# Optimization experiments

Measured on AMD Instinct MI355X. Metric: run time of the kernel, lower is better.

## Reference

```python
import jax, jax.numpy as jnp
import numpy as np

N_EMBED = 8192
EMB_DIM = 32
BETA = 1.0
DECAY = 0.99
N_TOKENS = 32768


def l2norm(x, axis=-1):
    # matches torch F.normalize(p=2, dim=-1, eps=1e-12)
    n = jnp.sqrt(jnp.sum(x * x, axis=axis, keepdims=True))
    return x / jnp.maximum(n, 1e-12)


def setup_inputs() -> dict:
    key = jax.random.key(0)
    k1, k2 = jax.random.split(key)
    z = jax.random.normal(k1, (N_TOKENS, EMB_DIM), dtype=jnp.float32)
    weight = l2norm(jax.random.normal(k2, (N_EMBED, EMB_DIM), dtype=jnp.float32))
    cluster_size = jnp.zeros((N_EMBED,), dtype=jnp.float32)
    return {"z": z, "weight": weight, "cluster_size": cluster_size}


def reference(z, weight, cluster_size):
    z = l2norm(z)  # [B, D]
    # pairwise squared L2 distances: [B, N]
    d = (jnp.sum(z * z, axis=1, keepdims=True)
         + jnp.sum(weight * weight, axis=1)
         - 2.0 * jnp.einsum('bd,nd->bn', z, weight))
    encoding_indices = jnp.argmin(d, axis=1)  # [B]
    z_q = weight[encoding_indices]            # gather, [B, D]

    # training-branch EMA updates (expressed functionally)
    bins = jnp.zeros((N_EMBED,), z.dtype).at[encoding_indices].add(1.0)
    new_cluster_size = cluster_size * DECAY + bins * (1.0 - DECAY)
    zero_mask = bins == 0
    safe_bins = jnp.where(zero_mask, 1.0, bins)
    # embed_sum = z^T @ one_hot(idx) done as a scatter-add: [N, D]
    embed_sum = jnp.zeros((N_EMBED, EMB_DIM), z.dtype).at[encoding_indices].add(z)
    embed_normalized = l2norm(embed_sum / safe_bins[:, None])
    embed_normalized = jnp.where(zero_mask[:, None], weight, embed_normalized)
    new_weight = l2norm(weight * DECAY + embed_normalized * (1.0 - DECAY))

    # commitment loss: z_q detached vs z
    loss = BETA * jnp.mean((jax.lax.stop_gradient(z_q) - z) ** 2)
    # straight-through estimator
    z_q_st = z + jax.lax.stop_gradient(z_q - z)
    return z_q_st, loss, encoding_indices, new_weight, new_cluster_size
```

## Files before the change

### kernel.cpp

```cpp
#include <hip/hip_runtime.h>
#include <math.h>

#define N_TOKENS 32768
#define N_EMBED  8192
#define EMB      32
#define DECAYF   0.99f
#define OMDF     0.01f

#define WS_WW    0
#define WS_ENC   (WS_WW + N_EMBED)
#define WS_BINS  (WS_ENC + N_TOKENS)
#define WS_ESUM  (WS_BINS + N_EMBED)
#define WS_LOSS  (WS_ESUM + N_EMBED*EMB)

#define OUT_ZQ   0
#define OUT_LOSS (N_TOKENS*EMB)
#define OUT_IDX  (OUT_LOSS + 1)
#define OUT_NW   (OUT_IDX + N_TOKENS)
#define OUT_CS   (OUT_NW + N_EMBED*EMB)

__global__ void k_prep(const float* __restrict__ z, const float* __restrict__ w,
                       float* __restrict__ zn, float* __restrict__ ww) {
    int t = blockIdx.x * blockDim.x + threadIdx.x;
    if (t < N_TOKENS) {
        const float4* zp = (const float4*)(z + (size_t)t * EMB);
        float4 v[8];
        float acc = 0.f;
#pragma unroll
        for (int i = 0; i < 8; ++i) {
            v[i] = zp[i];
            acc += v[i].x * v[i].x + v[i].y * v[i].y + v[i].z * v[i].z + v[i].w * v[i].w;
        }
        float n = fmaxf(sqrtf(acc), 1e-12f);
        float4* o = (float4*)(zn + (size_t)t * EMB);
#pragma unroll
        for (int i = 0; i < 8; ++i) {
            float4 r;
            r.x = v[i].x / n; r.y = v[i].y / n; r.z = v[i].z / n; r.w = v[i].w / n;
            o[i] = r;
        }
    } else if (t < N_TOKENS + N_EMBED) {
        int r = t - N_TOKENS;
        const float4* wp = (const float4*)(w + (size_t)r * EMB);
        float acc = 0.f;
#pragma unroll
        for (int i = 0; i < 8; ++i) {
            float4 v = wp[i];
            acc += v.x * v.x + v.y * v.y + v.z * v.z + v.w * v.w;
        }
        ww[r] = acc;
    }
}

#define SLICES 8
#define ROWS_PER_SLICE (N_EMBED / SLICES)

__global__ __launch_bounds__(512) void k_argmin(const float* __restrict__ zn,
                                                const float* __restrict__ weight,
                                                const float* __restrict__ ww,
                                                int* __restrict__ enc) {
    __shared__ float sBest[SLICES][64];
    __shared__ int   sIdx[SLICES][64];

    const int lane = threadIdx.x & 63;
    const int wv   = __builtin_amdgcn_readfirstlane(threadIdx.x >> 6);
    const int token = blockIdx.x * 64 + lane;

    float zr[EMB];
    const float4* zp = (const float4*)(zn + (size_t)token * EMB);
#pragma unroll
    for (int i = 0; i < 8; ++i) {
        float4 v = zp[i];
        zr[4 * i + 0] = v.x; zr[4 * i + 1] = v.y; zr[4 * i + 2] = v.z; zr[4 * i + 3] = v.w;
    }

    const int n0 = wv * ROWS_PER_SLICE;
    const float* wrow  = weight + (size_t)n0 * EMB;
    const float* wwrow = ww + n0;

    float best = 3.4e38f;
    int bidx = 0;

#pragma unroll 4
    for (int i = 0; i < ROWS_PER_SLICE; ++i) {
        const float4* wp = (const float4*)(wrow + (size_t)i * EMB);
        float a0 = 0.f, a1 = 0.f;
#pragma unroll
        for (int k = 0; k < 8; ++k) {
            float4 w4 = wp[k];
            a0 = fmaf(zr[4 * k + 0], w4.x, a0);
            a1 = fmaf(zr[4 * k + 1], w4.y, a1);
            a0 = fmaf(zr[4 * k + 2], w4.z, a0);
            a1 = fmaf(zr[4 * k + 3], w4.w, a1);
        }
        float key = fmaf(-2.f, a0 + a1, wwrow[i]);
        bool c = key < best;
        best = c ? key : best;
        bidx = c ? (n0 + i) : bidx;
    }

    sBest[wv][lane] = best;
    sIdx[wv][lane]  = bidx;
    __syncthreads();

    if (wv == 0) {
        float b = sBest[0][lane];
        int   bi = sIdx[0][lane];
#pragma unroll
        for (int s = 1; s < SLICES; ++s) {
            float ob = sBest[s][lane];
            int   oi = sIdx[s][lane];
            bool c = ob < b;
            b  = c ? ob : b;
            bi = c ? oi : bi;
        }
        enc[token] = bi;
    }
}

__global__ void k_token(const float* __restrict__ weight,
                        const int* __restrict__ enc, float* __restrict__ out,
                        float* __restrict__ bins, float* __restrict__ esum,
                        float* __restrict__ loss) {
    int t = blockIdx.x * blockDim.x + threadIdx.x;
    int idx = enc[t];
    float4* zq = (float4*)(out + OUT_ZQ + (size_t)t * EMB);
    const float4* wp = (const float4*)(weight + (size_t)idx * EMB);

    float lacc = 0.f;
#pragma unroll
    for (int i = 0; i < 8; ++i) {
        float4 zv = zq[i];
        float4 wv = wp[i];
        float4 d, o;
        d.x = wv.x - zv.x; d.y = wv.y - zv.y; d.z = wv.z - zv.z; d.w = wv.w - zv.w;
        lacc += d.x * d.x + d.y * d.y + d.z * d.z + d.w * d.w;
        o.x = zv.x + d.x; o.y = zv.y + d.y; o.z = zv.z + d.z; o.w = zv.w + d.w;
        zq[i] = o;
        atomicAdd(esum + (size_t)idx * EMB + 4 * i + 0, zv.x);
        atomicAdd(esum + (size_t)idx * EMB + 4 * i + 1, zv.y);
        atomicAdd(esum + (size_t)idx * EMB + 4 * i + 2, zv.z);
        atomicAdd(esum + (size_t)idx * EMB + 4 * i + 3, zv.w);
    }
    out[OUT_IDX + t] = (float)idx;
    atomicAdd(bins + idx, 1.0f);

#pragma unroll
    for (int off = 32; off > 0; off >>= 1) lacc += __shfl_xor(lacc, off, 64);
    if ((threadIdx.x & 63) == 0) atomicAdd(loss, lacc);
}

__global__ void k_ema(const float* __restrict__ weight, const float* __restrict__ cs,
                      const float* __restrict__ bins, const float* __restrict__ esum,
                      const float* __restrict__ loss, float* __restrict__ out) {
    int n = blockIdx.x * blockDim.x + threadIdx.x;
    if (n == 0) {
        out[OUT_LOSS] = loss[0] * (1.0f / (float)(N_TOKENS * EMB));
    }
    if (n >= N_EMBED) return;

    float b = bins[n];
    out[OUT_CS + n] = cs[n] * DECAYF + b * OMDF;

    bool zero = (b == 0.0f);
    float safe = zero ? 1.0f : b;

    float w[EMB], en[EMB];
    const float* wrow = weight + (size_t)n * EMB;
    const float* erow = esum + (size_t)n * EMB;
    float nacc = 0.f;
#pragma unroll
    for (int i = 0; i < EMB; ++i) {
        w[i] = wrow[i];
        en[i] = erow[i] / safe;
        nacc += en[i] * en[i];
    }
    float nn = fmaxf(sqrtf(nacc), 1e-12f);
#pragma unroll
    for (int i = 0; i < EMB; ++i) {
        en[i] = zero ? w[i] : (en[i] / nn);
    }
    float acc2 = 0.f;
    float nw[EMB];
#pragma unroll
    for (int i = 0; i < EMB; ++i) {
        nw[i] = w[i] * DECAYF + en[i] * OMDF;
        acc2 += nw[i] * nw[i];
    }
    float n2 = fmaxf(sqrtf(acc2), 1e-12f);
#pragma unroll
    for (int i = 0; i < EMB; ++i) {
        out[OUT_NW + (size_t)n * EMB + i] = nw[i] / n2;
    }
}

extern "C" void kernel_launch(void* const* d_in, const int* in_sizes, int n_in,
                              void* d_out, int out_size, void* d_ws, size_t ws_size,
                              hipStream_t stream) {
    const float* z  = (const float*)d_in[0];
    const float* w  = (const float*)d_in[1];
    const float* cs = (const float*)d_in[2];
    float* out = (float*)d_out;
    float* ws  = (float*)d_ws;

    float* zn   = out + OUT_ZQ;
    float* ww   = ws + WS_WW;
    int*   enc  = (int*)(ws + WS_ENC);
    float* bins = ws + WS_BINS;
    float* esum = ws + WS_ESUM;
    float* loss = ws + WS_LOSS;

    hipMemsetAsync(bins, 0, (size_t)(N_EMBED + N_EMBED * EMB + 1) * sizeof(float), stream);

    k_prep<<<(N_TOKENS + N_EMBED + 255) / 256, 256, 0, stream>>>(z, w, zn, ww);
    k_argmin<<<N_TOKENS / 64, 512, 0, stream>>>(zn, w, ww, enc);
    k_token<<<N_TOKENS / 256, 256, 0, stream>>>(w, enc, out, bins, esum, loss);
    k_ema<<<(N_EMBED + 255) / 256, 256, 0, stream>>>(w, cs, bins, esum, loss, out);
}
```

Measured before the change: 396.8 us.

## Register-block two tokens per thread in argmin and fuse z normalization

The argmin kernel now has each lane handle two tokens, so every codebook row it loads feeds twice as many FMAs, halving codebook load traffic per token. The block grows to 1024 threads split into 16 codebook slices. Token L2 normalization moves from the prep kernel into the argmin kernel, where wave 0 writes zn, and the prep kernel shrinks to computing codebook norms. The cost is higher register pressure from two 32-float token vectors per thread, which may reduce occupancy under launch_bounds(1024,4).

```diff
diff --git a/kernel.cpp b/kernel.cpp
--- a/kernel.cpp
+++ b/kernel.cpp
@@ -19,102 +19,122 @@
 #define OUT_NW   (OUT_IDX + N_TOKENS)
 #define OUT_CS   (OUT_NW + N_EMBED*EMB)
 
-__global__ void k_prep(const float* __restrict__ z, const float* __restrict__ w,
-                       float* __restrict__ zn, float* __restrict__ ww) {
-    int t = blockIdx.x * blockDim.x + threadIdx.x;
-    if (t < N_TOKENS) {
-        const float4* zp = (const float4*)(z + (size_t)t * EMB);
-        float4 v[8];
-        float acc = 0.f;
-#pragma unroll
-        for (int i = 0; i < 8; ++i) {
-            v[i] = zp[i];
-            acc += v[i].x * v[i].x + v[i].y * v[i].y + v[i].z * v[i].z + v[i].w * v[i].w;
-        }
-        float n = fmaxf(sqrtf(acc), 1e-12f);
-        float4* o = (float4*)(zn + (size_t)t * EMB);
-#pragma unroll
-        for (int i = 0; i < 8; ++i) {
-            float4 r;
-            r.x = v[i].x / n; r.y = v[i].y / n; r.z = v[i].z / n; r.w = v[i].w / n;
-            o[i] = r;
-        }
-    } else if (t < N_TOKENS + N_EMBED) {
-        int r = t - N_TOKENS;
-        const float4* wp = (const float4*)(w + (size_t)r * EMB);
-        float acc = 0.f;
-#pragma unroll
-        for (int i = 0; i < 8; ++i) {
-            float4 v = wp[i];
-            acc += v.x * v.x + v.y * v.y + v.z * v.z + v.w * v.w;
-        }
-        ww[r] = acc;
-    }
-}
-
-#define SLICES 8
+__global__ void k_ww(const float* __restrict__ w, float* __restrict__ ww) {
+    int r = blockIdx.x * blockDim.x + threadIdx.x;
+    if (r >= N_EMBED) return;
+    const float4* wp = (const float4*)(w + (size_t)r * EMB);
+    float acc = 0.f;
+#pragma unroll
+    for (int i = 0; i < 8; ++i) {
+        float4 v = wp[i];
+        acc += v.x * v.x + v.y * v.y + v.z * v.z + v.w * v.w;
+    }
+    ww[r] = acc;
+}
+
+#define SLICES 16
 #define ROWS_PER_SLICE (N_EMBED / SLICES)
-
-__global__ __launch_bounds__(512) void k_argmin(const float* __restrict__ zn,
-                                                const float* __restrict__ weight,
-                                                const float* __restrict__ ww,
-                                                int* __restrict__ enc) {
-    __shared__ float sBest[SLICES][64];
-    __shared__ int   sIdx[SLICES][64];
+#define TOK_PER_BLOCK  128
+
+__global__ __launch_bounds__(1024, 4) void k_argmin(
+        const float* __restrict__ z, const float* __restrict__ weight,
+        const float* __restrict__ ww, int* __restrict__ enc,
+        float* __restrict__ zn) {
+    __shared__ float sBest[SLICES][2][64];
+    __shared__ int   sIdx[SLICES][2][64];
 
     const int lane = threadIdx.x & 63;
     const int wv   = __builtin_amdgcn_readfirstlane(threadIdx.x >> 6);
-    const int token = blockIdx.x * 64 + lane;
-
-    float zr[EMB];
-    const float4* zp = (const float4*)(zn + (size_t)token * EMB);
-#pragma unroll
-    for (int i = 0; i < 8; ++i) {
-        float4 v = zp[i];
-        zr[4 * i + 0] = v.x; zr[4 * i + 1] = v.y; zr[4 * i + 2] = v.z; zr[4 * i + 3] = v.w;
-    }
-
-    const int n0 = wv * ROWS_PER_SLICE;
-    const float* wrow  = weight + (size_t)n0 * EMB;
-    const float* wwrow = ww + n0;
-
-    float best = 3.4e38f;
-    int bidx = 0;
+    const int tok0 = blockIdx.x * TOK_PER_BLOCK + lane;
+    const int tok1 = tok0 + 64;
+
+    float zr0[EMB], zr1[EMB];
+    {
+        const float4* zp0 = (const float4*)(z + (size_t)tok0 * EMB);
+        const float4* zp1 = (const float4*)(z + (size_t)tok1 * EMB);
+        float acc0 = 0.f, acc1 = 0.f;
+#pragma unroll
+        for (int i = 0; i < 8; ++i) {
+            float4 v0 = zp0[i];
+            float4 v1 = zp1[i];
+            acc0 += v0.x * v0.x + v0.y * v0.y + v0.z * v0.z + v0.w * v0.w;
+            acc1 += v1.x * v1.x + v1.y * v1.y + v1.z * v1.z + v1.w * v1.w;
+            zr0[4*i+0] = v0.x; zr0[4*i+1] = v0.y; zr0[4*i+2] = v0.z; zr0[4*i+3] = v0.w;
+            zr1[4*i+0] = v1.x; zr1[4*i+1] = v1.y; zr1[4*i+2] = v1.z; zr1[4*i+3] = v1.w;
+        }
+        float n0 = fmaxf(sqrtf(acc0), 1e-12f);
+        float n1 = fmaxf(sqrtf(acc1), 1e-12f);
+#pragma unroll
+        for (int k = 0; k < EMB; ++k) { zr0[k] = zr0[k] / n0; zr1[k] = zr1[k] / n1; }
+    }
+#pragma unroll
+    for (int k = 0; k < EMB; ++k) {
+        asm volatile("" : "+v"(zr0[k]));
+        asm volatile("" : "+v"(zr1[k]));
+    }
+
+    if (wv == 0) {
+        float4* o0 = (float4*)(zn + (size_t)tok0 * EMB);
+        float4* o1 = (float4*)(zn + (size_t)tok1 * EMB);
+#pragma unroll
+        for (int i = 0; i < 8; ++i) {
+            float4 a, b;
+            a.x = zr0[4*i+0]; a.y = zr0[4*i+1]; a.z = zr0[4*i+2]; a.w = zr0[4*i+3];
+            b.x = zr1[4*i+0]; b.y = zr1[4*i+1]; b.z = zr1[4*i+2]; b.w = zr1[4*i+3];
+            o0[i] = a; o1[i] = b;
+        }
+    }
+
+    const int n0r = wv * ROWS_PER_SLICE;
+    const float* wrow  = weight + (size_t)n0r * EMB;
+    const float* wwrow = ww + n0r;
+
+    float best0 = 3.4e38f, best1 = 3.4e38f;
+    int bidx0 = 0, bidx1 = 0;
 
 #pragma unroll 4
     for (int i = 0; i < ROWS_PER_SLICE; ++i) {
         const float4* wp = (const float4*)(wrow + (size_t)i * EMB);
-        float a0 = 0.f, a1 = 0.f;
+        float a00 = 0.f, a01 = 0.f, a10 = 0.f, a11 = 0.f;
 #pragma unroll
         for (int k = 0; k < 8; ++k) {
             float4 w4 = wp[k];
-            a0 = fmaf(zr[4 * k + 0], w4.x, a0);
-            a1 = fmaf(zr[4 * k + 1], w4.y, a1);
-            a0 = fmaf(zr[4 * k + 2], w4.z, a0);
-            a1 = fmaf(zr[4 * k + 3], w4.w, a1);
-        }
-        float key = fmaf(-2.f, a0 + a1, wwrow[i]);
-        bool c = key < best;
-        best = c ? key : best;
-        bidx = c ? (n0 + i) : bidx;
-    }
-
-    sBest[wv][lane] = best;
-    sIdx[wv][lane]  = bidx;
+            a00 = fmaf(zr0[4*k+0], w4.x, a00);
+            a01 = fmaf(zr0[4*k+1], w4.y, a01);
+            a10 = fmaf(zr1[4*k+0], w4.x, a10);
+            a11 = fmaf(zr1[4*k+1], w4.y, a11);
+            a00 = fmaf(zr0[4*k+2], w4.z, a00);
+            a01 = fmaf(zr0[4*k+3], w4.w, a01);
+            a10 = fmaf(zr1[4*k+2], w4.z, a10);
+            a11 = fmaf(zr1[4*k+3], w4.w, a11);
+        }
+        float wwv = wwrow[i];
+        float key0 = fmaf(-2.f, a00 + a01, wwv);
+        float key1 = fmaf(-2.f, a10 + a11, wwv);
+        bool c0 = key0 < best0;
+        bool c1 = key1 < best1;
+        best0 = c0 ? key0 : best0;  bidx0 = c0 ? (n0r + i) : bidx0;
+        best1 = c1 ? key1 : best1;  bidx1 = c1 ? (n0r + i) : bidx1;
+    }
+
+    sBest[wv][0][lane] = best0;  sIdx[wv][0][lane] = bidx0;
+    sBest[wv][1][lane] = best1;  sIdx[wv][1][lane] = bidx1;
     __syncthreads();
 
-    if (wv == 0) {
-        float b = sBest[0][lane];
-        int   bi = sIdx[0][lane];
+    if (threadIdx.x < 2 * 64) {
+        const int l = threadIdx.x & 63;
+        const int t = threadIdx.x >> 6;
+        float b = sBest[0][t][l];
+        int   bi = sIdx[0][t][l];
 #pragma unroll
         for (int s = 1; s < SLICES; ++s) {
-            float ob = sBest[s][lane];
-            int   oi = sIdx[s][lane];
+            float ob = sBest[s][t][l];
+            int   oi = sIdx[s][t][l];
             bool c = ob < b;
             b  = c ? ob : b;
             bi = c ? oi : bi;
         }
-        enc[token] = bi;
+        enc[blockIdx.x * TOK_PER_BLOCK + t * 64 + l] = bi;
     }
 }
 
@@ -212,8 +232,8 @@
 
     hipMemsetAsync(bins, 0, (size_t)(N_EMBED + N_EMBED * EMB + 1) * sizeof(float), stream);
 
-    k_prep<<<(N_TOKENS + N_EMBED + 255) / 256, 256, 0, stream>>>(z, w, zn, ww);
-    k_argmin<<<N_TOKENS / 64, 512, 0, stream>>>(zn, w, ww, enc);
+    k_ww<<<N_EMBED / 256, 256, 0, stream>>>(w, ww);
+    k_argmin<<<N_TOKENS / TOK_PER_BLOCK, 1024, 0, stream>>>(z, w, ww, enc, zn);
     k_token<<<N_TOKENS / 256, 256, 0, stream>>>(w, enc, out, bins, esum, loss);
     k_ema<<<(N_EMBED + 255) / 256, 256, 0, stream>>>(w, cs, bins, esum, loss, out);
 }
```

Measured after the change: 357.0 us. 10.0% less time.

## Restructure argmin so each lane holds a codebook row and waves share 16 tokens

Applied to the files above, without the earlier changes.

The argmin kernel is reorganised. Each lane now keeps one codebook row in registers, and each wave loops over all codebook chunks for 16 tokens whose normalized values are read as wave-uniform (scalar) loads. Weight rows are double-buffered in registers so the next chunk loads while the current one is computed, and per-token winners are reduced with cross-lane shuffles, with a tie-break on lower index. The normalized z is moved into the workspace and the weight-norm computation gets its own kernel. The goal is to cut the per-token reloading of the whole codebook and raise arithmetic reuse, at the cost of much higher register pressure from the waves_per_eu(2,2) hint and far fewer blocks.

```diff
diff --git a/kernel.cpp b/kernel.cpp
--- a/kernel.cpp
+++ b/kernel.cpp
@@ -7,7 +7,8 @@
 #define DECAYF   0.99f
 #define OMDF     0.01f
 
-#define WS_WW    0
+#define WS_ZN    0
+#define WS_WW    (N_TOKENS*EMB)
 #define WS_ENC   (WS_WW + N_EMBED)
 #define WS_BINS  (WS_ENC + N_TOKENS)
 #define WS_ESUM  (WS_BINS + N_EMBED)
@@ -19,124 +20,142 @@
 #define OUT_NW   (OUT_IDX + N_TOKENS)
 #define OUT_CS   (OUT_NW + N_EMBED*EMB)
 
-__global__ void k_prep(const float* __restrict__ z, const float* __restrict__ w,
-                       float* __restrict__ zn, float* __restrict__ ww) {
+__global__ void k_prep(const float* __restrict__ z, float* __restrict__ zn) {
     int t = blockIdx.x * blockDim.x + threadIdx.x;
-    if (t < N_TOKENS) {
-        const float4* zp = (const float4*)(z + (size_t)t * EMB);
-        float4 v[8];
-        float acc = 0.f;
-#pragma unroll
-        for (int i = 0; i < 8; ++i) {
-            v[i] = zp[i];
-            acc += v[i].x * v[i].x + v[i].y * v[i].y + v[i].z * v[i].z + v[i].w * v[i].w;
-        }
-        float n = fmaxf(sqrtf(acc), 1e-12f);
-        float4* o = (float4*)(zn + (size_t)t * EMB);
-#pragma unroll
-        for (int i = 0; i < 8; ++i) {
-            float4 r;
-            r.x = v[i].x / n; r.y = v[i].y / n; r.z = v[i].z / n; r.w = v[i].w / n;
-            o[i] = r;
-        }
-    } else if (t < N_TOKENS + N_EMBED) {
-        int r = t - N_TOKENS;
-        const float4* wp = (const float4*)(w + (size_t)r * EMB);
-        float acc = 0.f;
-#pragma unroll
-        for (int i = 0; i < 8; ++i) {
-            float4 v = wp[i];
-            acc += v.x * v.x + v.y * v.y + v.z * v.z + v.w * v.w;
-        }
-        ww[r] = acc;
-    }
-}
-
-#define SLICES 8
-#define ROWS_PER_SLICE (N_EMBED / SLICES)
-
-__global__ __launch_bounds__(512) void k_argmin(const float* __restrict__ zn,
-                                                const float* __restrict__ weight,
-                                                const float* __restrict__ ww,
-                                                int* __restrict__ enc) {
-    __shared__ float sBest[SLICES][64];
-    __shared__ int   sIdx[SLICES][64];
-
+    const float4* zp = (const float4*)(z + (size_t)t * EMB);
+    float4 v[8];
+    float acc = 0.f;
+#pragma unroll
+    for (int i = 0; i < 8; ++i) {
+        v[i] = zp[i];
+        acc += v[i].x * v[i].x + v[i].y * v[i].y + v[i].z * v[i].z + v[i].w * v[i].w;
+    }
+    float n = fmaxf(sqrtf(acc), 1e-12f);
+    float4* o = (float4*)(zn + (size_t)t * EMB);
+#pragma unroll
+    for (int i = 0; i < 8; ++i) {
+        float4 r;
+        r.x = v[i].x / n; r.y = v[i].y / n; r.z = v[i].z / n; r.w = v[i].w / n;
+        o[i] = r;
+    }
+}
+
+__global__ void k_ww(const float* __restrict__ w, float* __restrict__ ww) {
+    int r = blockIdx.x * blockDim.x + threadIdx.x;
+    if (r >= N_EMBED) return;
+    const float4* wp = (const float4*)(w + (size_t)r * EMB);
+    float acc = 0.f;
+#pragma unroll
+    for (int i = 0; i < 8; ++i) {
+        float4 v = wp[i];
+        acc += v.x * v.x + v.y * v.y + v.z * v.z + v.w * v.w;
+    }
+    ww[r] = acc;
+}
+
+#define TOKS_PER_WAVE 16
+#define WAVES_PER_BLOCK 8
+#define CHUNKS (N_EMBED / 64)
+
+#define LOADW(BUF, CC) do {                                                    \
+    const float4* wp_ = (const float4*)(weight + ((size_t)((CC) * 64 + lane)) * EMB); \
+    _Pragma("unroll")                                                          \
+    for (int q_ = 0; q_ < 8; ++q_) {                                           \
+        float4 v_ = wp_[q_];                                                   \
+        BUF[4*q_+0] = v_.x; BUF[4*q_+1] = v_.y;                                \
+        BUF[4*q_+2] = v_.z; BUF[4*q_+3] = v_.w;                                \
+    }                                                                          \
+} while (0)
+
+#define COMPUTE(W, WWV, CC) do {                                               \
+    const int rowbase_ = (CC) * 64 + lane;                                     \
+    _Pragma("unroll")                                                          \
+    for (int t_ = 0; t_ < TOKS_PER_WAVE; ++t_) {                               \
+        const float* zt_ = zb + t_ * EMB;                                      \
+        float d0_ = 0.f, d1_ = 0.f, d2_ = 0.f, d3_ = 0.f;                      \
+        _Pragma("unroll")                                                      \
+        for (int k_ = 0; k_ < 8; ++k_) {                                       \
+            d0_ = fmaf(W[4*k_+0], zt_[4*k_+0], d0_);                           \
+            d1_ = fmaf(W[4*k_+1], zt_[4*k_+1], d1_);                           \
+            d2_ = fmaf(W[4*k_+2], zt_[4*k_+2], d2_);                           \
+            d3_ = fmaf(W[4*k_+3], zt_[4*k_+3], d3_);                           \
+        }                                                                      \
+        float key_ = fmaf(-2.f, (d0_ + d1_) + (d2_ + d3_), WWV);               \
+        bool c_ = key_ < best[t_];           \
+        best[t_] = c_ ? key_ : best[t_];                                       \
+        bidx[t_] = c_ ? rowbase_ : bidx[t_];                                   \
+    }                                                                          \
+} while (0)
+
+__global__ __attribute__((amdgpu_flat_work_group_size(512, 512),
+                          amdgpu_waves_per_eu(2, 2)))
+void k_argmin(const float* __restrict__ zn, const float* __restrict__ weight,
+              const float* __restrict__ ww, int* __restrict__ enc) {
     const int lane = threadIdx.x & 63;
     const int wv   = __builtin_amdgcn_readfirstlane(threadIdx.x >> 6);
-    const int token = blockIdx.x * 64 + lane;
-
-    float zr[EMB];
-    const float4* zp = (const float4*)(zn + (size_t)token * EMB);
-#pragma unroll
-    for (int i = 0; i < 8; ++i) {
-        float4 v = zp[i];
-        zr[4 * i + 0] = v.x; zr[4 * i + 1] = v.y; zr[4 * i + 2] = v.z; zr[4 * i + 3] = v.w;
-    }
-
-    const int n0 = wv * ROWS_PER_SLICE;
-    const float* wrow  = weight + (size_t)n0 * EMB;
-    const float* wwrow = ww + n0;
-
-    float best = 3.4e38f;
-    int bidx = 0;
-
-#pragma unroll 4
-    for (int i = 0; i < ROWS_PER_SLICE; ++i) {
-        const float4* wp = (const float4*)(wrow + (size_t)i * EMB);
-        float a0 = 0.f, a1 = 0.f;
-#pragma unroll
-        for (int k = 0; k < 8; ++k) {
-            float4 w4 = wp[k];
-            a0 = fmaf(zr[4 * k + 0], w4.x, a0);
-            a1 = fmaf(zr[4 * k + 1], w4.y, a1);
-            a0 = fmaf(zr[4 * k + 2], w4.z, a0);
-            a1 = fmaf(zr[4 * k + 3], w4.w, a1);
+    const int wid  = blockIdx.x * WAVES_PER_BLOCK + wv;
+    const int tok0 = wid * TOKS_PER_WAVE;
+    const float* zb = zn + (size_t)tok0 * EMB;
+
+    float best[TOKS_PER_WAVE];
+    int   bidx[TOKS_PER_WAVE];
+#pragma unroll
+    for (int t = 0; t < TOKS_PER_WAVE; ++t) { best[t] = 3.4e38f; bidx[t] = 0; }
+
+    float wA[32], wB[32];
+    float wwA, wwB;
+
+    LOADW(wA, 0);
+    wwA = ww[lane];
+
+#pragma unroll 1
+    for (int c = 0; c < CHUNKS; c += 2) {
+        LOADW(wB, c + 1);
+        wwB = ww[(c + 1) * 64 + lane];
+        COMPUTE(wA, wwA, c);
+
+        const int cn = (c + 2 < CHUNKS) ? (c + 2) : 0;
+        LOADW(wA, cn);
+        wwA = ww[cn * 64 + lane];
+        COMPUTE(wB, wwB, c + 1);
+    }
+
+#pragma unroll
+    for (int t = 0; t < TOKS_PER_WAVE; ++t) {
+        float b = best[t];
+        int   bi = bidx[t];
+#pragma unroll
+        for (int off = 32; off >= 1; off >>= 1) {
+            float ob = __shfl_xor(b, off, 64);
+            int   oi = __shfl_xor(bi, off, 64);
+            bool c2 = (ob < b) || (ob == b && oi < bi);
+            b  = c2 ? ob : b;
+            bi = c2 ? oi : bi;
         }
-        float key = fmaf(-2.f, a0 + a1, wwrow[i]);
-        bool c = key < best;
-        best = c ? key : best;
-        bidx = c ? (n0 + i) : bidx;
-    }
-
-    sBest[wv][lane] = best;
-    sIdx[wv][lane]  = bidx;
-    __syncthreads();
-
-    if (wv == 0) {
-        float b = sBest[0][lane];
-        int   bi = sIdx[0][lane];
-#pragma unroll
-        for (int s = 1; s < SLICES; ++s) {
-            float ob = sBest[s][lane];
-            int   oi = sIdx[s][lane];
-            bool c = ob < b;
-            b  = c ? ob : b;
-            bi = c ? oi : bi;
-        }
-        enc[token] = bi;
-    }
-}
-
-__global__ void k_token(const float* __restrict__ weight,
+        if (lane == 0) enc[tok0 + t] = bi;
+    }
+}
+
+__global__ void k_token(const float* __restrict__ zn, const float* __restrict__ weight,
                         const int* __restrict__ enc, float* __restrict__ out,
                         float* __restrict__ bins, float* __restrict__ esum,
                         float* __restrict__ loss) {
     int t = blockIdx.x * blockDim.x + threadIdx.x;
     int idx = enc[t];
-    float4* zq = (float4*)(out + OUT_ZQ + (size_t)t * EMB);
+    const float4* zp = (const float4*)(zn + (size_t)t * EMB);
     const float4* wp = (const float4*)(weight + (size_t)idx * EMB);
+    float4* oq = (float4*)(out + OUT_ZQ + (size_t)t * EMB);
 
     float lacc = 0.f;
 #pragma unroll
     for (int i = 0; i < 8; ++i) {
-        float4 zv = zq[i];
+        float4 zv = zp[i];
         float4 wv = wp[i];
         float4 d, o;
         d.x = wv.x - zv.x; d.y = wv.y - zv.y; d.z = wv.z - zv.z; d.w = wv.w - zv.w;
         lacc += d.x * d.x + d.y * d.y + d.z * d.z + d.w * d.w;
         o.x = zv.x + d.x; o.y = zv.y + d.y; o.z = zv.z + d.z; o.w = zv.w + d.w;
-        zq[i] = o;
+        oq[i] = o;
         atomicAdd(esum + (size_t)idx * EMB + 4 * i + 0, zv.x);
         atomicAdd(esum + (size_t)idx * EMB + 4 * i + 1, zv.y);
         atomicAdd(esum + (size_t)idx * EMB + 4 * i + 2, zv.z);
@@ -203,7 +222,7 @@
     float* out = (float*)d_out;
     float* ws  = (float*)d_ws;
 
-    float* zn   = out + OUT_ZQ;
+    float* zn   = ws + WS_ZN;
     float* ww   = ws + WS_WW;
     int*   enc  = (int*)(ws + WS_ENC);
     float* bins = ws + WS_BINS;
@@ -212,8 +231,9 @@
 
     hipMemsetAsync(bins, 0, (size_t)(N_EMBED + N_EMBED * EMB + 1) * sizeof(float), stream);
 
-    k_prep<<<(N_TOKENS + N_EMBED + 255) / 256, 256, 0, stream>>>(z, w, zn, ww);
-    k_argmin<<<N_TOKENS / 64, 512, 0, stream>>>(zn, w, ww, enc);
-    k_token<<<N_TOKENS / 256, 256, 0, stream>>>(w, enc, out, bins, esum, loss);
+    k_prep<<<N_TOKENS / 256, 256, 0, stream>>>(z, zn);
+    k_ww<<<N_EMBED / 256, 256, 0, stream>>>(w, ww);
+    k_argmin<<<N_TOKENS / (TOKS_PER_WAVE * WAVES_PER_BLOCK), 512, 0, stream>>>(zn, w, ww, enc);
+    k_token<<<N_TOKENS / 256, 256, 0, stream>>>(zn, w, enc, out, bins, esum, loss);
     k_ema<<<(N_EMBED + 255) / 256, 256, 0, stream>>>(w, cs, bins, esum, loss, out);
 }
```

Result: slower. 881.7 us (+122.2%).

## Use split-bf16 MFMA distance scan with exact fp32 candidate re-check

Applied to the files above, without the earlier changes.

Replaces the scalar fp32 argmin over all codebook rows with a matrix-core scan that uses hi/lo bf16 splits (three MFMAs per tile) to approximate the dot products. A first pass picks an approximate best index. An exact fp32 key for that index then sets a per-token threshold, and a second scan records every candidate within epsilon of it. The candidates are re-scored exactly and merged with a packed 64-bit atomicMin. This trades the full fp32 FMA workload for two MFMA passes plus a small exact correction. It adds risk from the candidate buffer cap, atomic contention, and the epsilon margin being enough to preserve exact argmin ties.

```diff
diff --git a/kernel.cpp b/kernel.cpp
--- a/kernel.cpp
+++ b/kernel.cpp
@@ -6,12 +6,23 @@
 #define EMB      32
 #define DECAYF   0.99f
 #define OMDF     0.01f
-
-#define WS_WW    0
-#define WS_ENC   (WS_WW + N_EMBED)
-#define WS_BINS  (WS_ENC + N_TOKENS)
-#define WS_ESUM  (WS_BINS + N_EMBED)
-#define WS_LOSS  (WS_ESUM + N_EMBED*EMB)
+#define EPSK     2e-4f
+#define CAND_CAP 65536
+
+typedef unsigned short ushortT;
+typedef __attribute__((ext_vector_type(8))) short short8;
+typedef __attribute__((ext_vector_type(4))) float f32x4;
+
+#define WS_WHI  0
+#define WS_WLO  (WS_WHI + 131072)
+#define WS_WWN  (WS_WLO + 131072)
+#define WS_THR  (WS_WWN + N_EMBED)
+#define WS_PACK (WS_THR + N_TOKENS)
+#define WS_BINS (WS_PACK + 2*N_TOKENS)
+#define WS_ESUM (WS_BINS + N_EMBED)
+#define WS_LOSS (WS_ESUM + N_EMBED*EMB)
+#define WS_CCNT (WS_LOSS + 1)
+#define WS_CAND (WS_CCNT + 1)
 
 #define OUT_ZQ   0
 #define OUT_LOSS (N_TOKENS*EMB)
@@ -19,132 +30,272 @@
 #define OUT_NW   (OUT_IDX + N_TOKENS)
 #define OUT_CS   (OUT_NW + N_EMBED*EMB)
 
-__global__ void k_prep(const float* __restrict__ z, const float* __restrict__ w,
-                       float* __restrict__ zn, float* __restrict__ ww) {
-    int t = blockIdx.x * blockDim.x + threadIdx.x;
-    if (t < N_TOKENS) {
-        const float4* zp = (const float4*)(z + (size_t)t * EMB);
-        float4 v[8];
-        float acc = 0.f;
-#pragma unroll
-        for (int i = 0; i < 8; ++i) {
-            v[i] = zp[i];
-            acc += v[i].x * v[i].x + v[i].y * v[i].y + v[i].z * v[i].z + v[i].w * v[i].w;
-        }
-        float n = fmaxf(sqrtf(acc), 1e-12f);
-        float4* o = (float4*)(zn + (size_t)t * EMB);
-#pragma unroll
-        for (int i = 0; i < 8; ++i) {
-            float4 r;
-            r.x = v[i].x / n; r.y = v[i].y / n; r.z = v[i].z / n; r.w = v[i].w / n;
-            o[i] = r;
-        }
-    } else if (t < N_TOKENS + N_EMBED) {
-        int r = t - N_TOKENS;
-        const float4* wp = (const float4*)(w + (size_t)r * EMB);
-        float acc = 0.f;
-#pragma unroll
-        for (int i = 0; i < 8; ++i) {
-            float4 v = wp[i];
-            acc += v.x * v.x + v.y * v.y + v.z * v.z + v.w * v.w;
-        }
-        ww[r] = acc;
-    }
-}
-
-#define SLICES 8
-#define ROWS_PER_SLICE (N_EMBED / SLICES)
-
-__global__ __launch_bounds__(512) void k_argmin(const float* __restrict__ zn,
-                                                const float* __restrict__ weight,
-                                                const float* __restrict__ ww,
-                                                int* __restrict__ enc) {
-    __shared__ float sBest[SLICES][64];
-    __shared__ int   sIdx[SLICES][64];
-
-    const int lane = threadIdx.x & 63;
-    const int wv   = __builtin_amdgcn_readfirstlane(threadIdx.x >> 6);
-    const int token = blockIdx.x * 64 + lane;
-
-    float zr[EMB];
-    const float4* zp = (const float4*)(zn + (size_t)token * EMB);
+__device__ __forceinline__ ushortT bf16rn(float x) {
+    unsigned b = __float_as_uint(x);
+    unsigned r = (b + 0x7FFFu + ((b >> 16) & 1u)) >> 16;
+    return (ushortT)r;
+}
+__device__ __forceinline__ float bf16tof(ushortT u) {
+    return __uint_as_float(((unsigned)u) << 16);
+}
+__device__ __forceinline__ void load_zn_row(const float* __restrict__ z, int t, float* zr) {
+    const float4* zp = (const float4*)(z + (size_t)t * EMB);
+    float acc = 0.f;
 #pragma unroll
     for (int i = 0; i < 8; ++i) {
         float4 v = zp[i];
-        zr[4 * i + 0] = v.x; zr[4 * i + 1] = v.y; zr[4 * i + 2] = v.z; zr[4 * i + 3] = v.w;
-    }
-
-    const int n0 = wv * ROWS_PER_SLICE;
-    const float* wrow  = weight + (size_t)n0 * EMB;
-    const float* wwrow = ww + n0;
-
-    float best = 3.4e38f;
-    int bidx = 0;
-
-#pragma unroll 4
-    for (int i = 0; i < ROWS_PER_SLICE; ++i) {
-        const float4* wp = (const float4*)(wrow + (size_t)i * EMB);
-        float a0 = 0.f, a1 = 0.f;
-#pragma unroll
-        for (int k = 0; k < 8; ++k) {
-            float4 w4 = wp[k];
-            a0 = fmaf(zr[4 * k + 0], w4.x, a0);
-            a1 = fmaf(zr[4 * k + 1], w4.y, a1);
-            a0 = fmaf(zr[4 * k + 2], w4.z, a0);
-            a1 = fmaf(zr[4 * k + 3], w4.w, a1);
+        zr[4*i+0] = v.x; zr[4*i+1] = v.y; zr[4*i+2] = v.z; zr[4*i+3] = v.w;
+        acc += v.x*v.x + v.y*v.y + v.z*v.z + v.w*v.w;
+    }
+    float n = fmaxf(sqrtf(acc), 1e-12f);
+#pragma unroll
+    for (int k = 0; k < EMB; ++k) zr[k] = zr[k] / n;
+}
+__device__ __forceinline__ float exact_key(const float* zr, const float* __restrict__ wrow, float ww) {
+    float d0 = 0.f, d1 = 0.f, d2 = 0.f, d3 = 0.f;
+#pragma unroll
+    for (int k = 0; k < 8; ++k) {
+        d0 = fmaf(zr[4*k+0], wrow[4*k+0], d0);
+        d1 = fmaf(zr[4*k+1], wrow[4*k+1], d1);
+        d2 = fmaf(zr[4*k+2], wrow[4*k+2], d2);
+        d3 = fmaf(zr[4*k+3], wrow[4*k+3], d3);
+    }
+    return fmaf(-2.f, (d0 + d1) + (d2 + d3), ww);
+}
+__device__ __forceinline__ unsigned long long packkey(float k, int idx) {
+    unsigned u = __float_as_uint(k);
+    u = (u & 0x80000000u) ? ~u : (u | 0x80000000u);
+    return (((unsigned long long)u) << 32) | (unsigned)idx;
+}
+
+__global__ void k_prep(const float* __restrict__ z, ushortT* __restrict__ zhi,
+                       ushortT* __restrict__ zlo) {
+    int t = blockIdx.x * blockDim.x + threadIdx.x;
+    float zr[EMB];
+    load_zn_row(z, t, zr);
+    unsigned h[16], l[16];
+#pragma unroll
+    for (int i = 0; i < 16; ++i) {
+        ushortT h0 = bf16rn(zr[2*i]), h1 = bf16rn(zr[2*i+1]);
+        float r0 = zr[2*i] - bf16tof(h0), r1 = zr[2*i+1] - bf16tof(h1);
+        ushortT l0 = bf16rn(r0), l1 = bf16rn(r1);
+        h[i] = (unsigned)h0 | ((unsigned)h1 << 16);
+        l[i] = (unsigned)l0 | ((unsigned)l1 << 16);
+    }
+    uint4* dh = (uint4*)(zhi + (size_t)t * EMB);
+    uint4* dl = (uint4*)(zlo + (size_t)t * EMB);
+#pragma unroll
+    for (int q = 0; q < 4; ++q) {
+        dh[q] = make_uint4(h[4*q], h[4*q+1], h[4*q+2], h[4*q+3]);
+        dl[q] = make_uint4(l[4*q], l[4*q+1], l[4*q+2], l[4*q+3]);
+    }
+}
+
+__global__ void k_wprep(const float* __restrict__ w, ushortT* __restrict__ whi,
+                        ushortT* __restrict__ wlo, float* __restrict__ wwn) {
+    int r = blockIdx.x * blockDim.x + threadIdx.x;
+    if (r >= N_EMBED) return;
+    const float4* wp = (const float4*)(w + (size_t)r * EMB);
+    float wr[EMB];
+    float acc = 0.f;
+#pragma unroll
+    for (int i = 0; i < 8; ++i) {
+        float4 v = wp[i];
+        wr[4*i+0] = v.x; wr[4*i+1] = v.y; wr[4*i+2] = v.z; wr[4*i+3] = v.w;
+        acc += v.x*v.x + v.y*v.y + v.z*v.z + v.w*v.w;
+    }
+    wwn[r] = -0.5f * acc;
+    unsigned h[16], l[16];
+#pragma unroll
+    for (int i = 0; i < 16; ++i) {
+        ushortT h0 = bf16rn(wr[2*i]), h1 = bf16rn(wr[2*i+1]);
+        float r0 = wr[2*i] - bf16tof(h0), r1 = wr[2*i+1] - bf16tof(h1);
+        ushortT l0 = bf16rn(r0), l1 = bf16rn(r1);
+        h[i] = (unsigned)h0 | ((unsigned)h1 << 16);
+        l[i] = (unsigned)l0 | ((unsigned)l1 << 16);
+    }
+    uint4* dh = (uint4*)(whi + (size_t)r * EMB);
+    uint4* dl = (uint4*)(wlo + (size_t)r * EMB);
+#pragma unroll
+    for (int q = 0; q < 4; ++q) {
+        dh[q] = make_uint4(h[4*q], h[4*q+1], h[4*q+2], h[4*q+3]);
+        dl[q] = make_uint4(l[4*q], l[4*q+1], l[4*q+2], l[4*q+3]);
+    }
+}
+
+template<int MODE>
+__global__ __launch_bounds__(256) void k_scan(
+        const ushortT* __restrict__ zhi, const ushortT* __restrict__ zlo,
+        const ushortT* __restrict__ whi, const ushortT* __restrict__ wlo,
+        const float* __restrict__ wwn, const float* __restrict__ thr,
+        unsigned long long* __restrict__ packed,
+        unsigned* __restrict__ ccnt, unsigned long long* __restrict__ cand) {
+    const int lane = threadIdx.x & 63;
+    const int wv   = threadIdx.x >> 6;
+    const int wid  = blockIdx.x * 4 + wv;
+    const int tok0 = wid * 32;
+    const int l15  = lane & 15;
+    const int lg   = lane >> 4;
+
+    const size_t aoff0 = ((size_t)(tok0 + l15)) * EMB + 8 * lg;
+    const size_t aoff1 = ((size_t)(tok0 + 16 + l15)) * EMB + 8 * lg;
+    const short8 a0h = *(const short8*)(zhi + aoff0);
+    const short8 a0l = *(const short8*)(zlo + aoff0);
+    const short8 a1h = *(const short8*)(zhi + aoff1);
+    const short8 a1l = *(const short8*)(zlo + aoff1);
+
+    float best0[4], best1[4];
+    int   bid0[4], bid1[4];
+    float thrv0[4], thrv1[4];
+    if (MODE == 0) {
+#pragma unroll
+        for (int r = 0; r < 4; ++r) {
+            best0[r] = -3.4e38f; best1[r] = -3.4e38f; bid0[r] = 0; bid1[r] = 0;
         }
-        float key = fmaf(-2.f, a0 + a1, wwrow[i]);
-        bool c = key < best;
-        best = c ? key : best;
-        bidx = c ? (n0 + i) : bidx;
-    }
-
-    sBest[wv][lane] = best;
-    sIdx[wv][lane]  = bidx;
-    __syncthreads();
-
-    if (wv == 0) {
-        float b = sBest[0][lane];
-        int   bi = sIdx[0][lane];
-#pragma unroll
-        for (int s = 1; s < SLICES; ++s) {
-            float ob = sBest[s][lane];
-            int   oi = sIdx[s][lane];
-            bool c = ob < b;
-            b  = c ? ob : b;
-            bi = c ? oi : bi;
+    } else {
+#pragma unroll
+        for (int r = 0; r < 4; ++r) {
+            thrv0[r] = thr[tok0 + lg * 4 + r];
+            thrv1[r] = thr[tok0 + 16 + lg * 4 + r];
         }
-        enc[token] = bi;
-    }
-}
-
-__global__ void k_token(const float* __restrict__ weight,
-                        const int* __restrict__ enc, float* __restrict__ out,
-                        float* __restrict__ bins, float* __restrict__ esum,
-                        float* __restrict__ loss) {
+    }
+
+    int vn = l15;
+#pragma unroll 2
+    for (int nt = 0; nt < N_EMBED / 16; ++nt) {
+        const size_t boff = ((size_t)(nt * 16 + l15)) * EMB + 8 * lg;
+        const short8 bh = *(const short8*)(whi + boff);
+        const short8 bl = *(const short8*)(wlo + boff);
+        const float cv = wwn[nt * 16 + l15];
+        f32x4 c0 = {cv, cv, cv, cv};
+        f32x4 c1 = {cv, cv, cv, cv};
+        c0 = __builtin_amdgcn_mfma_f32_16x16x32_bf16(a0l, bh, c0, 0, 0, 0);
+        c0 = __builtin_amdgcn_mfma_f32_16x16x32_bf16(a0h, bl, c0, 0, 0, 0);
+        c0 = __builtin_amdgcn_mfma_f32_16x16x32_bf16(a0h, bh, c0, 0, 0, 0);
+        c1 = __builtin_amdgcn_mfma_f32_16x16x32_bf16(a1l, bh, c1, 0, 0, 0);
+        c1 = __builtin_amdgcn_mfma_f32_16x16x32_bf16(a1h, bl, c1, 0, 0, 0);
+        c1 = __builtin_amdgcn_mfma_f32_16x16x32_bf16(a1h, bh, c1, 0, 0, 0);
+
+        if (MODE == 0) {
+#pragma unroll
+            for (int r = 0; r < 4; ++r) {
+                bool g0 = c0[r] > best0[r];
+                best0[r] = g0 ? c0[r] : best0[r];
+                bid0[r]  = g0 ? vn : bid0[r];
+                bool g1 = c1[r] > best1[r];
+                best1[r] = g1 ? c1[r] : best1[r];
+                bid1[r]  = g1 ? vn : bid1[r];
+            }
+        } else {
+            float k0[4], k1[4];
+#pragma unroll
+            for (int r = 0; r < 4; ++r) { k0[r] = -2.f * c0[r]; k1[r] = -2.f * c1[r]; }
+            bool f = (k0[0] <= thrv0[0]) | (k0[1] <= thrv0[1]) | (k0[2] <= thrv0[2]) |
+                     (k0[3] <= thrv0[3]) | (k1[0] <= thrv1[0]) | (k1[1] <= thrv1[1]) |
+                     (k1[2] <= thrv1[2]) | (k1[3] <= thrv1[3]);
+            if (f) {
+#pragma unroll
+                for (int r = 0; r < 4; ++r) {
+                    if (k0[r] <= thrv0[r]) {
+                        unsigned slot = atomicAdd(ccnt, 1u);
+                        if (slot < CAND_CAP)
+                            cand[slot] = (((unsigned long long)(unsigned)(tok0 + lg*4 + r)) << 32) | (unsigned)vn;
+                    }
+                    if (k1[r] <= thrv1[r]) {
+                        unsigned slot = atomicAdd(ccnt, 1u);
+                        if (slot < CAND_CAP)
+                            cand[slot] = (((unsigned long long)(unsigned)(tok0 + 16 + lg*4 + r)) << 32) | (unsigned)vn;
+                    }
+                }
+            }
+        }
+        vn += 16;
+    }
+
+    if (MODE == 0) {
+#pragma unroll
+        for (int r = 0; r < 4; ++r) {
+            float b = best0[r]; int bi = bid0[r];
+#pragma unroll
+            for (int off = 1; off < 16; off <<= 1) {
+                float ob = __shfl_xor(b, off, 64);
+                int   oi = __shfl_xor(bi, off, 64);
+                bool c = (ob > b) || (ob == b && oi < bi);
+                b = c ? ob : b; bi = c ? oi : bi;
+            }
+            if (l15 == 0) packed[tok0 + lg * 4 + r] = packkey(-2.f * b, bi);
+
+            float b1 = best1[r]; int bi1 = bid1[r];
+#pragma unroll
+            for (int off = 1; off < 16; off <<= 1) {
+                float ob = __shfl_xor(b1, off, 64);
+                int   oi = __shfl_xor(bi1, off, 64);
+                bool c = (ob > b1) || (ob == b1 && oi < bi1);
+                b1 = c ? ob : b1; bi1 = c ? oi : bi1;
+            }
+            if (l15 == 0) packed[tok0 + 16 + lg * 4 + r] = packkey(-2.f * b1, bi1);
+        }
+    }
+}
+
+__global__ void k_exact(const float* __restrict__ z, const float* __restrict__ weight,
+                        const float* __restrict__ wwn,
+                        unsigned long long* __restrict__ packed, float* __restrict__ thr) {
     int t = blockIdx.x * blockDim.x + threadIdx.x;
-    int idx = enc[t];
-    float4* zq = (float4*)(out + OUT_ZQ + (size_t)t * EMB);
+    int idx = (int)(packed[t] & 0xFFFFFFFFull);
+    float zr[EMB];
+    load_zn_row(z, t, zr);
+    float key = exact_key(zr, weight + (size_t)idx * EMB, -2.f * wwn[idx]);
+    thr[t] = key + EPSK;
+    packed[t] = packkey(key, idx);
+}
+
+__global__ void k_resolve(const float* __restrict__ z, const float* __restrict__ weight,
+                          const float* __restrict__ wwn,
+                          const unsigned* __restrict__ ccnt,
+                          const unsigned long long* __restrict__ cand,
+                          unsigned long long* __restrict__ packed) {
+    unsigned i = blockIdx.x * blockDim.x + threadIdx.x;
+    unsigned n = *ccnt;
+    if (n > CAND_CAP) n = CAND_CAP;
+    if (i >= n) return;
+    unsigned long long e = cand[i];
+    int tok = (int)(e >> 32);
+    int row = (int)(e & 0xFFFFFFFFull);
+    float zr[EMB];
+    load_zn_row(z, tok, zr);
+    float key = exact_key(zr, weight + (size_t)row * EMB, -2.f * wwn[row]);
+    atomicMin(packed + tok, packkey(key, row));
+}
+
+__global__ void k_token(const float* __restrict__ z, const float* __restrict__ weight,
+                        const unsigned long long* __restrict__ packed,
+                        float* __restrict__ out, float* __restrict__ bins,
+                        float* __restrict__ esum, float* __restrict__ loss) {
+    int t = blockIdx.x * blockDim.x + threadIdx.x;
+    int idx = (int)(packed[t] & 0xFFFFFFFFull);
+    float zr[EMB];
+    load_zn_row(z, t, zr);
     const float4* wp = (const float4*)(weight + (size_t)idx * EMB);
+    float4* oq = (float4*)(out + OUT_ZQ + (size_t)t * EMB);
 
     float lacc = 0.f;
 #pragma unroll
     for (int i = 0; i < 8; ++i) {
-        float4 zv = zq[i];
         float4 wv = wp[i];
+        float zx = zr[4*i+0], zy = zr[4*i+1], zz2 = zr[4*i+2], zw = zr[4*i+3];
         float4 d, o;
-        d.x = wv.x - zv.x; d.y = wv.y - zv.y; d.z = wv.z - zv.z; d.w = wv.w - zv.w;
-        lacc += d.x * d.x + d.y * d.y + d.z * d.z + d.w * d.w;
-        o.x = zv.x + d.x; o.y = zv.y + d.y; o.z = zv.z + d.z; o.w = zv.w + d.w;
-        zq[i] = o;
-        atomicAdd(esum + (size_t)idx * EMB + 4 * i + 0, zv.x);
-        atomicAdd(esum + (size_t)idx * EMB + 4 * i + 1, zv.y);
-        atomicAdd(esum + (size_t)idx * EMB + 4 * i + 2, zv.z);
-        atomicAdd(esum + (size_t)idx * EMB + 4 * i + 3, zv.w);
+        d.x = wv.x - zx; d.y = wv.y - zy; d.z = wv.z - zz2; d.w = wv.w - zw;
+        lacc += d.x*d.x + d.y*d.y + d.z*d.z + d.w*d.w;
+        o.x = zx + d.x; o.y = zy + d.y; o.z = zz2 + d.z; o.w = zw + d.w;
+        oq[i] = o;
+        atomicAdd(esum + (size_t)idx * EMB + 4*i + 0, zx);
+        atomicAdd(esum + (size_t)idx * EMB + 4*i + 1, zy);
+        atomicAdd(esum + (size_t)idx * EMB + 4*i + 2, zz2);
+        atomicAdd(esum + (size_t)idx * EMB + 4*i + 3, zw);
     }
     out[OUT_IDX + t] = (float)idx;
     atomicAdd(bins + idx, 1.0f);
-
 #pragma unroll
     for (int off = 32; off > 0; off >>= 1) lacc += __shfl_xor(lacc, off, 64);
     if ((threadIdx.x & 63) == 0) atomicAdd(loss, lacc);
@@ -154,14 +305,11 @@
                       const float* __restrict__ bins, const float* __restrict__ esum,
                       const float* __restrict__ loss, float* __restrict__ out) {
     int n = blockIdx.x * blockDim.x + threadIdx.x;
-    if (n == 0) {
-        out[OUT_LOSS] = loss[0] * (1.0f / (float)(N_TOKENS * EMB));
-    }
+    if (n == 0) out[OUT_LOSS] = loss[0] * (1.0f / (float)(N_TOKENS * EMB));
     if (n >= N_EMBED) return;
 
     float b = bins[n];
     out[OUT_CS + n] = cs[n] * DECAYF + b * OMDF;
-
     bool zero = (b == 0.0f);
     float safe = zero ? 1.0f : b;
 
@@ -177,9 +325,7 @@
     }
     float nn = fmaxf(sqrtf(nacc), 1e-12f);
 #pragma unroll
-    for (int i = 0; i < EMB; ++i) {
-        en[i] = zero ? w[i] : (en[i] / nn);
-    }
+    for (int i = 0; i < EMB; ++i) en[i] = zero ? w[i] : (en[i] / nn);
     float acc2 = 0.f;
     float nw[EMB];
 #pragma unroll
@@ -189,9 +335,7 @@
     }
     float n2 = fmaxf(sqrtf(acc2), 1e-12f);
 #pragma unroll
-    for (int i = 0; i < EMB; ++i) {
-        out[OUT_NW + (size_t)n * EMB + i] = nw[i] / n2;
-    }
+    for (int i = 0; i < EMB; ++i) out[OUT_NW + (size_t)n * EMB + i] = nw[i] / n2;
 }
 
 extern "C" void kernel_launch(void* const* d_in, const int* in_sizes, int n_in,
@@ -203,17 +347,27 @@
     float* out = (float*)d_out;
     float* ws  = (float*)d_ws;
 
-    float* zn   = out + OUT_ZQ;
-    float* ww   = ws + WS_WW;
-    int*   enc  = (int*)(ws + WS_ENC);
+    ushortT* zhi = (ushortT*)(out + OUT_ZQ);
+    ushortT* zlo = zhi + (size_t)N_TOKENS * EMB;
+    ushortT* whi = (ushortT*)(ws + WS_WHI);
+    ushortT* wlo = (ushortT*)(ws + WS_WLO);
+    float* wwn  = ws + WS_WWN;
+    float* thr  = ws + WS_THR;
+    unsigned long long* packed = (unsigned long long*)(ws + WS_PACK);
     float* bins = ws + WS_BINS;
     float* esum = ws + WS_ESUM;
     float* loss = ws + WS_LOSS;
-
-    hipMemsetAsync(bins, 0, (size_t)(N_EMBED + N_EMBED * EMB + 1) * sizeof(float), stream);
-
-    k_prep<<<(N_TOKENS + N_EMBED + 255) / 256, 256, 0, stream>>>(z, w, zn, ww);
-    k_argmin<<<N_TOKENS / 64, 512, 0, stream>>>(zn, w, ww, enc);
-    k_token<<<N_TOKENS / 256, 256, 0, stream>>>(w, enc, out, bins, esum, loss);
-    k_ema<<<(N_EMBED + 255) / 256, 256, 0, stream>>>(w, cs, bins, esum, loss, out);
-}
+    unsigned* ccnt = (unsigned*)(ws + WS_CCNT);
+    unsigned long long* cand = (unsigned long long*)(ws + WS_CAND);
+
+    hipMemsetAsync(bins, 0, (size_t)(WS_CAND - WS_BINS) * sizeof(float), stream);
+
+    k_prep<<<N_TOKENS / 256, 256, 0, stream>>>(z, zhi, zlo);
+    k_wprep<<<N_EMBED / 256, 256, 0, stream>>>(w, whi, wlo, wwn);
+    k_scan<0><<<N_TOKENS / 128, 256, 0, stream>>>(zhi, zlo, whi, wlo, wwn, thr, packed, ccnt, cand);
+    k_exact<<<N_TOKENS / 256, 256, 0, stream>>>(z, w, wwn, packed, thr);
+    k_scan<1><<<N_TOKENS / 128, 256, 0, stream>>>(zhi, zlo, whi, wlo, wwn, thr, packed, ccnt, cand);
+    k_resolve<<<CAND_CAP / 256, 256, 0, stream>>>(z, w, wwn, ccnt, cand, packed);
+    k_token<<<N_TOKENS / 256, 256, 0, stream>>>(z, w, packed, out, bins, esum, loss);
+    k_ema<<<N_EMBED / 256, 256, 0, stream>>>(w, cs, bins, esum, loss, out);
+}
```

After: 758.6 us. 1.91x slower.
